# Performance work log

Measured on AMD Instinct MI355X. Metric: run time of the kernel, lower is better.

## Reference

```python
import jax, jax.numpy as jnp
import numpy as np

DIM = 2048
HID = 4096          # multiple_of*ceil(int(2*6144/3)/256)
STATE = 128
HEADS = 64
GROUPS = 1
CONV = 4
CHUNK = 256
HEAD_DIM = HID // HEADS            # 64
CONV_DIM = HID + 2 * GROUPS * STATE  # 4352
D_IN = 2 * HID + 2 * GROUPS * STATE + HEADS  # 8512


def setup_inputs() -> dict:
    key = jax.random.key(0)
    ks = jax.random.split(key, 8)
    x = jax.random.normal(ks[0], (1, 4096, DIM), dtype=jnp.float32)
    in_proj_w = jax.random.normal(ks[1], (D_IN, DIM), jnp.float32) * (DIM ** -0.5)
    conv_w = jax.random.normal(ks[2], (CONV_DIM, CONV), jnp.float32) * (CONV ** -0.5)
    # dt_bias init: log(expm1(uniform(dt_min, dt_max)))
    dt_bias = jnp.log(jnp.expm1(jax.random.uniform(ks[3], (HEADS,), jnp.float32, 0.001, 0.1)))
    # A_log init: log(uniform(A_init_min, A_init_max))
    A_log = jnp.log(jax.random.uniform(ks[4], (HEADS,), jnp.float32, 1.0, 16.0))
    D = jnp.ones((HEADS,), jnp.float32)
    norm_w = jnp.ones((HID,), jnp.float32)
    out_proj_w = jax.random.normal(ks[5], (DIM, HID), jnp.float32) * (HID ** -0.5)
    return dict(x=x, in_proj_w=in_proj_w, conv_w=conv_w, dt_bias=dt_bias,
                A_log=A_log, D=D, norm_w=norm_w, out_proj_w=out_proj_w)


def _causal_conv1d_silu(xBC, w):
    # xBC: (b, s, c); w: (c, k) depthwise causal conv, then SiLU
    b, s, c = xBC.shape
    k = w.shape[1]
    xp = jnp.pad(xBC, ((0, 0), (k - 1, 0), (0, 0)))
    out = xp[:, 0:s, :] * w[:, 0]
    for i in range(1, k):
        out = out + xp[:, i:i + s, :] * w[:, i]
    return jax.nn.silu(out)


def _ssd_chunk_scan(x, dt, A, B, C, D, chunk):
    # x: (b,s,h,p), dt: (b,s,h) post-softplus, A: (h,) negative, B,C: (b,s,g,n)
    b, s, h, p = x.shape
    g, n = B.shape[2], B.shape[3]
    c = s // chunk
    Bh = jnp.repeat(B, h // g, axis=2).reshape(b, c, chunk, h, n)
    Ch = jnp.repeat(C, h // g, axis=2).reshape(b, c, chunk, h, n)
    xr = x.reshape(b, c, chunk, h, p)
    dtr = dt.reshape(b, c, chunk, h)
    dA = dtr * A                      # (b,c,l,h)
    dAc = jnp.cumsum(dA, axis=2)      # (b,c,l,h)
    # intra-chunk (diagonal blocks): decay[i,j] = exp(dAc[i]-dAc[j]) for i>=j
    seg = dAc[:, :, :, None, :] - dAc[:, :, None, :, :]   # (b,c,l,l,h)
    mask = jnp.tril(jnp.ones((chunk, chunk), bool))
    Lmat = jnp.where(mask[None, None, :, :, None], jnp.exp(seg), 0.0)
    xdt = xr * dtr[..., None]         # dt-scaled inputs
    y_diag = jnp.einsum('bclhn,bcshn,bclsh,bcshp->bclhp', Ch, Bh, Lmat, xdt)
    # per-chunk end states
    dA_last = dAc[:, :, -1:, :]                       # (b,c,1,h)
    decay_states = jnp.exp(dA_last - dAc)             # (b,c,l,h)
    states = jnp.einsum('bclhn,bclh,bclhp->bchpn', Bh, decay_states, xdt)
    # inter-chunk recurrence
    chunk_decay = jnp.exp(dA_last[:, :, 0, :])        # (b,c,h)
    def step(carry, inp):
        dec, st = inp
        new = carry * dec[:, :, None, None] + st
        return new, carry
    init = jnp.zeros((b, h, p, n), x.dtype)
    _, prev = jax.lax.scan(step, init,
                           (jnp.moveaxis(chunk_decay, 1, 0), jnp.moveaxis(states, 1, 0)))
    prev = jnp.moveaxis(prev, 0, 1)                   # (b,c,h,p,n) state entering each chunk
    y_off = jnp.einsum('bclhn,bclh,bchpn->bclhp', Ch, jnp.exp(dAc), prev)
    y = (y_diag + y_off).reshape(b, s, h, p)
    return y + x * D[None, None, :, None]


def reference(x, in_proj_w, conv_w, dt_bias, A_log, D, norm_w, out_proj_w):
    b, s, _ = x.shape
    zxbcdt = x @ in_proj_w.T                          # (b,s,D_IN)
    z = zxbcdt[..., :HID]
    xBC = zxbcdt[..., HID:HID + CONV_DIM]
    dt = zxbcdt[..., HID + CONV_DIM:]                 # (b,s,heads)
    xBC = _causal_conv1d_silu(xBC, conv_w)
    xh = xBC[..., :HID].reshape(b, s, HEADS, HEAD_DIM)
    B = xBC[..., HID:HID + GROUPS * STATE].reshape(b, s, GROUPS, STATE)
    C = xBC[..., HID + GROUPS * STATE:].reshape(b, s, GROUPS, STATE)
    A = -jnp.exp(A_log)
    dt = jax.nn.softplus(dt + dt_bias)                # dt_softplus=True with dt_bias
    y = _ssd_chunk_scan(xh, dt, A, B, C, D, CHUNK)
    y = y.reshape(b, s, HID)
    y = y * jax.nn.silu(z)                            # gated
    y = y * jax.lax.rsqrt(jnp.mean(y * y, axis=-1, keepdims=True) + 1e-5) * norm_w
    return y @ out_proj_w.T
```

## Files before the change

### kernel.cpp

```cpp
#include <hip/hip_runtime.h>
#include <cstdint>
#include <cstddef>

#define SEQ      4096
#define DIMIN    2048
#define HID      4096
#define STATE    128
#define HEADS    64
#define HEAD_DIM 64
#define CONV_DIM 4352
#define D_IN     8512
#define WROWS    8576
#define XBCD_N   4480
#define CHUNK    256
#define NCHUNK   16

typedef __attribute__((ext_vector_type(8))) short short8;
typedef __attribute__((ext_vector_type(4))) float floatx4;
typedef __attribute__((ext_vector_type(4))) unsigned int uintx4;

#define AS1 __attribute__((address_space(1)))
#define AS3 __attribute__((address_space(3)))
__device__ __forceinline__ void gload_lds16(const void* g, void* l) {
    __builtin_amdgcn_global_load_lds((const AS1 unsigned int*)g, (AS3 unsigned int*)l, 16, 0, 0);
}

__device__ __forceinline__ unsigned short f2bf(float f) {
    union { float f; unsigned int u; } v; v.f = f;
    unsigned int r = v.u + 0x7FFFu + ((v.u >> 16) & 1u);
    return (unsigned short)(r >> 16);
}
__device__ __forceinline__ float bf2f(unsigned short u) {
    union { unsigned int u; float f; } v; v.u = ((unsigned int)u) << 16;
    return v.f;
}

__global__ void k_convert(const float* __restrict__ src, unsigned short* __restrict__ dst,
                          long n, long nsrc) {
    long i = (long)blockIdx.x * blockDim.x + threadIdx.x;
    if (i >= n) return;
    float v = (i < nsrc) ? src[i] : 0.f;
    dst[i] = f2bf(v);
}

#define BM 128
#define BN 128
#define BK 64

template <int BF16OUT>
__global__ __launch_bounds__(256) void k_gemm(
    const unsigned short* __restrict__ A, const unsigned short* __restrict__ B,
    void* __restrict__ Cout, int K, int ldc, float* __restrict__ aux, int auxc0)
{
    __shared__ __attribute__((aligned(16))) unsigned short As[BM * BK];
    __shared__ __attribute__((aligned(16))) unsigned short Bs[BN * BK];
    const int tid = threadIdx.x;

    const int GN = 8;
    const int nbx = gridDim.x, nby = gridDim.y;
    int flat = blockIdx.y * nbx + blockIdx.x;
    int group = flat / (GN * nby);
    int gw = min(GN, nbx - group * GN);
    int rem = flat - group * (GN * nby);
    int bn = group * GN + rem % gw;
    int bm = rem / gw;

    const int wid = tid >> 6, lane = tid & 63;
    const int wm = (wid >> 1) * 64, wn = (wid & 1) * 64;
    const int lrow = lane & 15;
    const int gk = lane >> 4;
    const int srow = lane >> 3;
    const int sgrp = (lane & 7) ^ (lane >> 3);

    floatx4 acc[4][4];
#pragma unroll
    for (int i = 0; i < 4; ++i)
#pragma unroll
        for (int j = 0; j < 4; ++j) acc[i][j] = (floatx4){0.f, 0.f, 0.f, 0.f};

    const long a_base = (long)bm * BM * K;
    const long b_base = (long)bn * BN * K;

    for (int k0 = 0; k0 < K; k0 += BK) {
        const unsigned short* Ak = A + a_base + k0;
        const unsigned short* Bk = B + b_base + k0;
#pragma unroll
        for (int i = 0; i < 4; ++i) {
            int rbase = wid * 32 + i * 8;
            gload_lds16(Ak + (long)(rbase + srow) * K + sgrp * 8, &As[rbase * BK]);
            gload_lds16(Bk + (long)(rbase + srow) * K + sgrp * 8, &Bs[rbase * BK]);
        }
        __syncthreads();
#pragma unroll
        for (int kk = 0; kk < BK; kk += 32) {
            const int slot8 = (((kk >> 3) + gk) ^ (lrow & 7)) * 8;
            short8 af[4], bfr[4];
#pragma unroll
            for (int i = 0; i < 4; ++i)
                af[i] = *(const short8*)&As[(wm + i * 16 + lrow) * BK + slot8];
#pragma unroll
            for (int j = 0; j < 4; ++j)
                bfr[j] = *(const short8*)&Bs[(wn + j * 16 + lrow) * BK + slot8];
#pragma unroll
            for (int i = 0; i < 4; ++i)
#pragma unroll
                for (int j = 0; j < 4; ++j)
                    acc[i][j] = __builtin_amdgcn_mfma_f32_16x16x32_bf16(af[i], bfr[j], acc[i][j], 0, 0, 0);
        }
        __syncthreads();
    }
    const int rcol = lane & 15;
    const int rrow = (lane >> 4) * 4;
#pragma unroll
    for (int i = 0; i < 4; ++i)
#pragma unroll
        for (int j = 0; j < 4; ++j) {
            int col = bn * BN + wn + j * 16 + rcol;
#pragma unroll
            for (int r = 0; r < 4; ++r) {
                int row = bm * BM + wm + i * 16 + rrow + r;
                float v = acc[i][j][r];
                if (BF16OUT) {
                    ((unsigned short*)Cout)[(long)row * ldc + col] = f2bf(v);
                    if (aux && col >= auxc0 && col < auxc0 + 64)
                        aux[(long)row * 64 + (col - auxc0)] = v;
                } else {
                    ((float*)Cout)[(long)row * ldc + col] = v;
                }
            }
        }
}

__global__ void k_conv(const unsigned short* __restrict__ xbcd, const float* __restrict__ convw,
                       unsigned short* __restrict__ xc) {
    long i = (long)blockIdx.x * 256 + threadIdx.x;
    if (i >= (long)SEQ * CONV_DIM) return;
    int c = (int)(i % CONV_DIM);
    int s = (int)(i / CONV_DIM);
    float w0 = convw[c * 4 + 0], w1 = convw[c * 4 + 1];
    float w2 = convw[c * 4 + 2], w3 = convw[c * 4 + 3];
    float acc = bf2f(xbcd[(long)s * XBCD_N + c]) * w3;
    if (s >= 1) acc += bf2f(xbcd[(long)(s - 1) * XBCD_N + c]) * w2;
    if (s >= 2) acc += bf2f(xbcd[(long)(s - 2) * XBCD_N + c]) * w1;
    if (s >= 3) acc += bf2f(xbcd[(long)(s - 3) * XBCD_N + c]) * w0;
    float sl = acc / (1.f + __expf(-acc));
    xc[i] = f2bf(sl);
}

__global__ __launch_bounds__(256) void k_dt(const float* __restrict__ dtraw,
        const float* __restrict__ dt_bias, const float* __restrict__ A_log,
        float* __restrict__ dtv, float* __restrict__ dAc, float* __restrict__ dAlast)
{
    int c = blockIdx.x, h = blockIdx.y;
    int l = threadIdx.x;
    __shared__ float sh[CHUNK];
    float v = dtraw[(long)(c * CHUNK + l) * 64 + h] + dt_bias[h];
    float dt = (v > 20.f) ? v : log1pf(__expf(v));
    float Ah = -__expf(A_log[h]);
    float dA = dt * Ah;
    sh[l] = dA;
    __syncthreads();
    float x = dA;
#pragma unroll
    for (int off = 1; off < CHUNK; off <<= 1) {
        float t = (l >= off) ? sh[l - off] : 0.f;
        __syncthreads();
        x += t;
        sh[l] = x;
        __syncthreads();
    }
    dtv[(long)(c * CHUNK + l) * HEADS + h] = dt;
    dAc[(long)(c * CHUNK + l) * HEADS + h] = x;
    if (l == CHUNK - 1) dAlast[c * HEADS + h] = x;
}

__global__ __launch_bounds__(256) void k_G(const unsigned short* __restrict__ xc, float* __restrict__ G) {
    int c = blockIdx.x, l = blockIdx.y;
    int s = threadIdx.x;
    __shared__ float Csh[STATE];
    if (s < STATE) Csh[s] = bf2f(xc[(long)(c * CHUNK + l) * CONV_DIM + HID + STATE + s]);
    __syncthreads();
    const unsigned short* Brow = xc + (long)(c * CHUNK + s) * CONV_DIM + HID;
    float acc = 0.f;
#pragma unroll
    for (int n = 0; n < STATE; n += 8) {
        short8 b8 = *(const short8*)&Brow[n];
#pragma unroll
        for (int j = 0; j < 8; ++j)
            acc += Csh[n + j] * bf2f((unsigned short)b8[j]);
    }
    G[((long)c * CHUNK + l) * CHUNK + s] = acc;
}

__global__ __launch_bounds__(256) void k_states(
    const unsigned short* __restrict__ xc, const float* __restrict__ dtv,
    const float* __restrict__ dAc, const float* __restrict__ dAlast,
    float* __restrict__ states)
{
    int c = blockIdx.x, h = blockIdx.y;
    int t = threadIdx.x;
    __shared__ float xs[64][64];
    __shared__ float dA_sh[CHUNK], dt_sh[CHUNK];
    long base_s = (long)c * CHUNK;
    dA_sh[t] = dAc[(base_s + t) * HEADS + h];
    dt_sh[t] = dtv[(base_s + t) * HEADS + h];
    __syncthreads();
    float dAl = dAlast[c * HEADS + h];
    int p0 = t >> 5;
    int n0 = t & 31;
    float acc[8][4];
#pragma unroll
    for (int ip = 0; ip < 8; ++ip)
#pragma unroll
        for (int j = 0; j < 4; ++j) acc[ip][j] = 0.f;

    for (int lb = 0; lb < 4; ++lb) {
#pragma unroll
        for (int i = 0; i < 16; ++i) {
            int e = t + i * 256;
            int r = e >> 6, pcol = e & 63;
            float ds = __expf(dAl - dA_sh[lb * 64 + r]) * dt_sh[lb * 64 + r];
            xs[r][pcol] = bf2f(xc[(base_s + lb * 64 + r) * CONV_DIM + h * HEAD_DIM + pcol]) * ds;
        }
        __syncthreads();
        for (int lp = 0; lp < 64; ++lp) {
            const unsigned short* Brow = xc + (base_s + lb * 64 + lp) * CONV_DIM + HID;
            float bv[4];
#pragma unroll
            for (int j = 0; j < 4; ++j) bv[j] = bf2f(Brow[n0 + 32 * j]);
#pragma unroll
            for (int ip = 0; ip < 8; ++ip) {
                float xv = xs[lp][p0 + 8 * ip];
#pragma unroll
                for (int j = 0; j < 4; ++j) acc[ip][j] += xv * bv[j];
            }
        }
        __syncthreads();
    }
    float* Sb = states + (long)(c * HEADS + h) * HEAD_DIM * STATE;
#pragma unroll
    for (int ip = 0; ip < 8; ++ip)
#pragma unroll
        for (int j = 0; j < 4; ++j)
            Sb[(p0 + 8 * ip) * STATE + n0 + 32 * j] = acc[ip][j];
}

__global__ void k_scan(float* __restrict__ states, const float* __restrict__ dAlast) {
    int t = blockIdx.x * 256 + threadIdx.x;
    if (t >= HEADS * HEAD_DIM * STATE) return;
    int h = t >> 13;
    const long stride = (long)HEADS * HEAD_DIM * STATE;
    float carry = 0.f;
    for (int c = 0; c < NCHUNK; ++c) {
        float s = states[c * stride + t];
        float dec = __expf(dAlast[c * HEADS + h]);
        states[c * stride + t] = carry;
        carry = carry * dec + s;
    }
}

#define XDTS 264
#define PVS  136
__global__ __launch_bounds__(256, 3) void k_ssd_y(
    const unsigned short* __restrict__ xc, const float* __restrict__ G,
    const float* __restrict__ dtv, const float* __restrict__ dAc,
    const float* __restrict__ prev, const float* __restrict__ Dp,
    unsigned short* __restrict__ y)
{
    __shared__ __attribute__((aligned(16))) unsigned short xdtT[64 * XDTS];
    __shared__ __attribute__((aligned(16))) unsigned short pvB[64 * PVS];
    __shared__ float dA_sh[CHUNK];
    __shared__ float dt_sh[CHUNK];
    const int c = blockIdx.x, h = blockIdx.y;
    const int t = threadIdx.x;
    const int w = t >> 6, lane = t & 63;
    const long base_s = (long)c * CHUNK;

    dA_sh[t] = dAc[(base_s + t) * HEADS + h];
    dt_sh[t] = dtv[(base_s + t) * HEADS + h];
    __syncthreads();

    {
        const float* Pb = prev + (long)(c * HEADS + h) * HEAD_DIM * STATE;
#pragma unroll
        for (int i = 0; i < 32; ++i) {
            int e = t + i * 256;
            int p = e >> 7, n = e & 127;
            pvB[p * PVS + n] = f2bf(Pb[e]);
        }
    }
#pragma unroll
    for (int i = 0; i < 64; ++i) {
        int e = t + i * 256;
        int p = e & 63, s = e >> 6;
        float v = bf2f(xc[(base_s + s) * CONV_DIM + h * HEAD_DIM + p]) * dt_sh[s];
        xdtT[p * XDTS + s] = f2bf(v);
    }
    __syncthreads();

    floatx4 acc[4][4];
#pragma unroll
    for (int i = 0; i < 4; ++i)
#pragma unroll
        for (int j = 0; j < 4; ++j) acc[i][j] = (floatx4){0.f, 0.f, 0.f, 0.f};

    const int lrow = lane & 15;
    const int kgrp = (lane >> 4) * 8;
    float myA[4], eAl[4];
#pragma unroll
    for (int i = 0; i < 4; ++i) {
        int l = w * 64 + i * 16 + lrow;
        myA[i] = dA_sh[l];
        eAl[i] = __expf(myA[i]);
    }

    for (int k0 = 0; k0 < STATE; k0 += 32) {
        short8 af[4], bfr[4];
#pragma unroll
        for (int i = 0; i < 4; ++i) {
            int l = w * 64 + i * 16 + lrow;
            union { short8 v; unsigned short u[8]; } r, o;
            r.v = *(const short8*)&xc[(base_s + l) * CONV_DIM + (HID + STATE) + k0 + kgrp];
#pragma unroll
            for (int j = 0; j < 8; ++j) o.u[j] = f2bf(bf2f(r.u[j]) * eAl[i]);
            af[i] = o.v;
        }
#pragma unroll
        for (int j = 0; j < 4; ++j)
            bfr[j] = *(const short8*)&pvB[(j * 16 + lrow) * PVS + k0 + kgrp];
#pragma unroll
        for (int i = 0; i < 4; ++i)
#pragma unroll
            for (int j = 0; j < 4; ++j)
                acc[i][j] = __builtin_amdgcn_mfma_f32_16x16x32_bf16(af[i], bfr[j], acc[i][j], 0, 0, 0);
    }

    for (int k0 = 0; k0 < (w + 1) * 64; k0 += 32) {
        short8 af[4], bfr[4];
#pragma unroll
        for (int i = 0; i < 4; ++i) {
            int l = w * 64 + i * 16 + lrow;
            const float* Gp = G + (base_s + l) * (long)CHUNK + k0 + kgrp;
            float4 g0 = *(const float4*)Gp;
            float4 g1 = *(const float4*)(Gp + 4);
            float ga[8] = {g0.x, g0.y, g0.z, g0.w, g1.x, g1.y, g1.z, g1.w};
            union { short8 v; unsigned short u[8]; } o;
#pragma unroll
            for (int j = 0; j < 8; ++j) {
                int s = k0 + kgrp + j;
                float e = __expf(fminf(myA[i] - dA_sh[s], 0.f));
                float m = (s <= l) ? ga[j] * e : 0.f;
                o.u[j] = f2bf(m);
            }
            af[i] = o.v;
        }
#pragma unroll
        for (int j = 0; j < 4; ++j)
            bfr[j] = *(const short8*)&xdtT[(j * 16 + lrow) * XDTS + k0 + kgrp];
#pragma unroll
        for (int i = 0; i < 4; ++i)
#pragma unroll
            for (int j = 0; j < 4; ++j)
                acc[i][j] = __builtin_amdgcn_mfma_f32_16x16x32_bf16(af[i], bfr[j], acc[i][j], 0, 0, 0);
    }

    const float Dh = Dp[h];
    const int rrow = (lane >> 4) * 4;
#pragma unroll
    for (int i = 0; i < 4; ++i)
#pragma unroll
        for (int j = 0; j < 4; ++j) {
            int p = j * 16 + lrow;
#pragma unroll
            for (int r = 0; r < 4; ++r) {
                int l = w * 64 + i * 16 + rrow + r;
                float v = acc[i][j][r] + Dh * bf2f(xc[(base_s + l) * CONV_DIM + h * HEAD_DIM + p]);
                y[(base_s + l) * (long)HID + h * HEAD_DIM + p] = f2bf(v);
            }
        }
}

__global__ __launch_bounds__(256) void k_norm(
    const unsigned short* __restrict__ y, const unsigned short* __restrict__ z,
    const float* __restrict__ norm_w, unsigned short* __restrict__ yb)
{
    int s = blockIdx.x;
    int t = threadIdx.x;
    const unsigned short* yrow = y + (long)s * HID;
    const unsigned short* zrow = z + (long)s * HID;
    float vals[16];
    float ss = 0.f;
#pragma unroll
    for (int i = 0; i < 16; ++i) {
        int j = t + i * 256;
        float yv = bf2f(yrow[j]);
        float zv = bf2f(zrow[j]);
        float g = yv * (zv / (1.f + __expf(-zv)));
        vals[i] = g;
        ss += g * g;
    }
#pragma unroll
    for (int off = 32; off > 0; off >>= 1) ss += __shfl_down(ss, off);
    __shared__ float wsum[4];
    int lane = t & 63, wid = t >> 6;
    if (lane == 0) wsum[wid] = ss;
    __syncthreads();
    float total = wsum[0] + wsum[1] + wsum[2] + wsum[3];
    float scale = rsqrtf(total / HID + 1e-5f);
#pragma unroll
    for (int i = 0; i < 16; ++i) {
        int j = t + i * 256;
        yb[(long)s * HID + j] = f2bf(vals[i] * scale * norm_w[j]);
    }
}

extern "C" void kernel_launch(void* const* d_in, const int* in_sizes, int n_in,
                              void* d_out, int out_size, void* d_ws, size_t ws_size,
                              hipStream_t stream) {
    const float* x          = (const float*)d_in[0];
    const float* in_proj_w  = (const float*)d_in[1];
    const float* conv_w     = (const float*)d_in[2];
    const float* dt_bias    = (const float*)d_in[3];
    const float* A_log      = (const float*)d_in[4];
    const float* Dp         = (const float*)d_in[5];
    const float* norm_w     = (const float*)d_in[6];
    const float* out_proj_w = (const float*)d_in[7];
    char* ws = (char*)d_ws;

    const size_t off_xb    = 0;
    const size_t off_wbin  = off_xb    + (size_t)SEQ * DIMIN * 2;
    const size_t off_xbcd  = off_wbin  + (size_t)WROWS * DIMIN * 2;
    const size_t off_xc    = off_xbcd  + (size_t)SEQ * XBCD_N * 2;
    const size_t off_dtraw = off_xc    + (size_t)SEQ * CONV_DIM * 2;
    const size_t off_dtv   = off_dtraw + (size_t)SEQ * 64 * 4;
    const size_t off_dAc   = off_dtv   + (size_t)SEQ * HEADS * 4;
    const size_t off_dAl   = off_dAc   + (size_t)SEQ * HEADS * 4;
    const size_t off_G     = off_dAl   + (size_t)NCHUNK * HEADS * 4;
    const size_t needed    = off_G     + (size_t)NCHUNK * CHUNK * CHUNK * 4;
    if (ws_size < needed) return;

    unsigned short* xb    = (unsigned short*)(ws + off_xb);
    unsigned short* wbin  = (unsigned short*)(ws + off_wbin);
    unsigned short* xbcd  = (unsigned short*)(ws + off_xbcd);
    unsigned short* xc    = (unsigned short*)(ws + off_xc);
    float* dtraw = (float*)(ws + off_dtraw);
    float* dtv   = (float*)(ws + off_dtv);
    float* dAc   = (float*)(ws + off_dAc);
    float* dAl   = (float*)(ws + off_dAl);
    float* G     = (float*)(ws + off_G);

    float* states      = (float*)d_out;
    unsigned short* z  = (unsigned short*)d_out;
    unsigned short* y  = xbcd;
    unsigned short* yb = xc;
    unsigned short* wob = wbin;

    { long n = (long)SEQ * DIMIN;
      k_convert<<<(unsigned)((n + 255) / 256), 256, 0, stream>>>(x, xb, n, n); }
    { long n = (long)WROWS * DIMIN, nsrc = (long)D_IN * DIMIN;
      k_convert<<<(unsigned)((n + 255) / 256), 256, 0, stream>>>(in_proj_w, wbin, n, nsrc); }
    k_gemm<1><<<dim3(XBCD_N / BN, SEQ / BM), 256, 0, stream>>>(
        xb, wbin + (size_t)HID * DIMIN, (void*)xbcd, DIMIN, XBCD_N, dtraw, 4352);
    { long n = (long)SEQ * CONV_DIM;
      k_conv<<<(unsigned)((n + 255) / 256), 256, 0, stream>>>(xbcd, conv_w, xc); }
    k_dt<<<dim3(NCHUNK, HEADS), 256, 0, stream>>>(dtraw, dt_bias, A_log, dtv, dAc, dAl);
    k_G<<<dim3(NCHUNK, CHUNK), 256, 0, stream>>>(xc, G);
    k_states<<<dim3(NCHUNK, HEADS), 256, 0, stream>>>(xc, dtv, dAc, dAl, states);
    k_scan<<<(HEADS * HEAD_DIM * STATE) / 256, 256, 0, stream>>>(states, dAl);
    k_ssd_y<<<dim3(NCHUNK, HEADS), 256, 0, stream>>>(xc, G, dtv, dAc, states, Dp, y);
    k_gemm<1><<<dim3(HID / BN, SEQ / BM), 256, 0, stream>>>(
        xb, wbin, (void*)z, DIMIN, HID, nullptr, 0);
    k_norm<<<SEQ, 256, 0, stream>>>(y, z, norm_w, yb);
    { long n = (long)DIMIN * HID;
      k_convert<<<(unsigned)((n + 255) / 256), 256, 0, stream>>>(out_proj_w, wob, n, n); }
    k_gemm<0><<<dim3(DIMIN / BN, SEQ / BM), 256, 0, stream>>>(
        yb, wob, d_out, HID, DIMIN, nullptr, 0);
}
```

Baseline: 766.7 us.

## Replace GEMM with 256x256 double-buffered pipelined kernel and split-K out_proj

Replaces the 128x128 single-buffered bf16 MFMA GEMM with a 256x256 tile, 512-thread kernel. It double-buffers LDS with interleaved global-to-LDS staging, raises wave priority around the MFMA blocks, and remaps workgroups to XCDs. The out_proj GEMM is split across K into two halves, with the second partial written to workspace and summed by a new add kernel. This targets low MFMA utilisation and load latency in all three GEMMs, and fills the GPU for the small out_proj grid. The cost is more LDS per block, an extra pass over the output, and tight barrier and vmcnt choreography that could misorder if counts are wrong.

```diff
diff --git a/kernel.cpp b/kernel.cpp
--- a/kernel.cpp
+++ b/kernel.cpp
@@ -17,7 +17,6 @@
 
 typedef __attribute__((ext_vector_type(8))) short short8;
 typedef __attribute__((ext_vector_type(4))) float floatx4;
-typedef __attribute__((ext_vector_type(4))) unsigned int uintx4;
 
 #define AS1 __attribute__((address_space(1)))
 #define AS3 __attribute__((address_space(3)))
@@ -43,92 +42,191 @@
     dst[i] = f2bf(v);
 }
 
-#define BM 128
-#define BN 128
-#define BK 64
+#define GBM 256
+#define GBN 256
+#define GBK 64
 
 template <int BF16OUT>
-__global__ __launch_bounds__(256) void k_gemm(
+__global__ __launch_bounds__(512, 2) void k_gemm256(
     const unsigned short* __restrict__ A, const unsigned short* __restrict__ B,
-    void* __restrict__ Cout, int K, int ldc, float* __restrict__ aux, int auxc0)
+    void* __restrict__ Cout, float* __restrict__ Cpart,
+    int Kloop, int ldk, int Nvalid, int ldc,
+    float* __restrict__ aux, int auxc0)
 {
-    __shared__ __attribute__((aligned(16))) unsigned short As[BM * BK];
-    __shared__ __attribute__((aligned(16))) unsigned short Bs[BN * BK];
-    const int tid = threadIdx.x;
-
-    const int GN = 8;
+    __shared__ __attribute__((aligned(16))) unsigned short As[2][GBM * GBK];
+    __shared__ __attribute__((aligned(16))) unsigned short Bs[2][GBN * GBK];
+
+    const int tid  = threadIdx.x;
+    const int wid  = tid >> 6, lane = tid & 63;
+    const int wm   = (wid >> 2) * 128;
+    const int wn   = (wid & 3) * 64;
+
     const int nbx = gridDim.x, nby = gridDim.y;
-    int flat = blockIdx.y * nbx + blockIdx.x;
-    int group = flat / (GN * nby);
-    int gw = min(GN, nbx - group * GN);
-    int rem = flat - group * (GN * nby);
-    int bn = group * GN + rem % gw;
-    int bm = rem / gw;
-
-    const int wid = tid >> 6, lane = tid & 63;
-    const int wm = (wid >> 1) * 64, wn = (wid & 1) * 64;
+    const int nwg = nbx * nby * (int)gridDim.z;
+    int flat = ((int)blockIdx.z * nby + blockIdx.y) * nbx + blockIdx.x;
+    int q = nwg >> 3, r = nwg & 7;
+    int xcd = flat & 7, loc = flat >> 3;
+    int f2 = (xcd < r ? xcd * (q + 1) : r * (q + 1) + (xcd - r) * q) + loc;
+    int bz  = f2 / (nbx * nby);
+    int rm2 = f2 - bz * nbx * nby;
+    int bm  = rm2 / nbx;
+    int bn  = rm2 % nbx;
+
+    const unsigned short* Ag = A + (long)bm * GBM * ldk + (long)bz * Kloop;
+    const unsigned short* Bg = B + (long)bn * GBN * ldk + (long)bz * Kloop;
+
+    const int s_r  = lane >> 3;
+    const int s_kg = (lane & 7) ^ s_r;
+
     const int lrow = lane & 15;
-    const int gk = lane >> 4;
-    const int srow = lane >> 3;
-    const int sgrp = (lane & 7) ^ (lane >> 3);
-
-    floatx4 acc[4][4];
-#pragma unroll
-    for (int i = 0; i < 4; ++i)
+    const int gk   = lane >> 4;
+
+    floatx4 acc[8][4];
+#pragma unroll
+    for (int i = 0; i < 8; ++i)
 #pragma unroll
         for (int j = 0; j < 4; ++j) acc[i][j] = (floatx4){0.f, 0.f, 0.f, 0.f};
 
-    const long a_base = (long)bm * BM * K;
-    const long b_base = (long)bn * BN * K;
-
-    for (int k0 = 0; k0 < K; k0 += BK) {
-        const unsigned short* Ak = A + a_base + k0;
-        const unsigned short* Bk = B + b_base + k0;
-#pragma unroll
-        for (int i = 0; i < 4; ++i) {
-            int rbase = wid * 32 + i * 8;
-            gload_lds16(Ak + (long)(rbase + srow) * K + sgrp * 8, &As[rbase * BK]);
-            gload_lds16(Bk + (long)(rbase + srow) * K + sgrp * 8, &Bs[rbase * BK]);
-        }
-        __syncthreads();
-#pragma unroll
-        for (int kk = 0; kk < BK; kk += 32) {
-            const int slot8 = (((kk >> 3) + gk) ^ (lrow & 7)) * 8;
-            short8 af[4], bfr[4];
-#pragma unroll
-            for (int i = 0; i < 4; ++i)
-                af[i] = *(const short8*)&As[(wm + i * 16 + lrow) * BK + slot8];
-#pragma unroll
-            for (int j = 0; j < 4; ++j)
-                bfr[j] = *(const short8*)&Bs[(wn + j * 16 + lrow) * BK + slot8];
-#pragma unroll
-            for (int i = 0; i < 4; ++i)
-#pragma unroll
-                for (int j = 0; j < 4; ++j)
-                    acc[i][j] = __builtin_amdgcn_mfma_f32_16x16x32_bf16(af[i], bfr[j], acc[i][j], 0, 0, 0);
-        }
-        __syncthreads();
-    }
-    const int rcol = lane & 15;
-    const int rrow = (lane >> 4) * 4;
-#pragma unroll
-    for (int i = 0; i < 4; ++i)
-#pragma unroll
-        for (int j = 0; j < 4; ++j) {
-            int col = bn * BN + wn + j * 16 + rcol;
-#pragma unroll
-            for (int r = 0; r < 4; ++r) {
-                int row = bm * BM + wm + i * 16 + rrow + r;
-                float v = acc[i][j][r];
+    short8 aLo[4][2], aHi[4][2], bF[4][2];
+
+    unsigned short* As0 = As[0]; unsigned short* Bs0 = Bs[0];
+    unsigned short* As1 = As[1]; unsigned short* Bs1 = Bs[1];
+
+    auto STAGE = [&](unsigned short* Ad, unsigned short* Bd, int tt, int p) {
+        long k0 = (long)tt * GBK;
+        if (k0 + GBK > Kloop) k0 = 0;
+        const int seg = p * 8 + wid;
+        const long ro = (long)(seg * 8 + s_r) * ldk + k0 + s_kg * 8;
+        gload_lds16(Ag + ro, Ad + seg * 512);
+        gload_lds16(Bg + ro, Bd + seg * 512);
+    };
+    auto LDA_ = [&](unsigned short* Asu, int m, int ks) -> short8 {
+        int row  = wm + m * 16 + lrow;
+        int slot = (gk + ks * 4) ^ (lrow & 7);
+        return *(const short8*)&Asu[row * 64 + slot * 8];
+    };
+    auto LDB_ = [&](unsigned short* Bsu, int n, int ks) -> short8 {
+        int row  = wn + n * 16 + lrow;
+        int slot = (gk + ks * 4) ^ (lrow & 7);
+        return *(const short8*)&Bsu[row * 64 + slot * 8];
+    };
+
+#pragma unroll
+    for (int p = 0; p < 4; ++p) STAGE(As0, Bs0, 0, p);
+    STAGE(As1, Bs1, 1, 0);
+    STAGE(As1, Bs1, 1, 1);
+    asm volatile("s_waitcnt vmcnt(4)" ::: "memory");
+    __builtin_amdgcn_s_barrier();
+    asm volatile("" ::: "memory");
+
+    const int nk = Kloop / GBK;
+
+    auto tile_step = [&](unsigned short* Asu, unsigned short* Bsu,
+                         unsigned short* AsN, unsigned short* BsN, int t) {
+#pragma unroll
+        for (int m = 0; m < 4; ++m) { aLo[m][0] = LDA_(Asu, m, 0); aLo[m][1] = LDA_(Asu, m, 1); }
+#pragma unroll
+        for (int n = 0; n < 2; ++n) { bF[n][0] = LDB_(Bsu, n, 0); bF[n][1] = LDB_(Bsu, n, 1); }
+        STAGE(AsN, BsN, t + 1, 2);
+        __builtin_amdgcn_s_barrier();
+        asm volatile("" ::: "memory");
+        __builtin_amdgcn_s_setprio(1);
+#pragma unroll
+        for (int m = 0; m < 4; ++m)
+#pragma unroll
+            for (int n = 0; n < 2; ++n)
+#pragma unroll
+                for (int ks = 0; ks < 2; ++ks)
+                    acc[m][n] = __builtin_amdgcn_mfma_f32_16x16x32_bf16(aLo[m][ks], bF[n][ks], acc[m][n], 0, 0, 0);
+        __builtin_amdgcn_s_setprio(0);
+        __builtin_amdgcn_s_barrier();
+        asm volatile("" ::: "memory");
+#pragma unroll
+        for (int n = 2; n < 4; ++n) { bF[n][0] = LDB_(Bsu, n, 0); bF[n][1] = LDB_(Bsu, n, 1); }
+        STAGE(AsN, BsN, t + 1, 3);
+        __builtin_amdgcn_s_barrier();
+        asm volatile("" ::: "memory");
+        __builtin_amdgcn_s_setprio(1);
+#pragma unroll
+        for (int m = 0; m < 4; ++m)
+#pragma unroll
+            for (int n = 2; n < 4; ++n)
+#pragma unroll
+                for (int ks = 0; ks < 2; ++ks)
+                    acc[m][n] = __builtin_amdgcn_mfma_f32_16x16x32_bf16(aLo[m][ks], bF[n][ks], acc[m][n], 0, 0, 0);
+        __builtin_amdgcn_s_setprio(0);
+        __builtin_amdgcn_s_barrier();
+        asm volatile("" ::: "memory");
+#pragma unroll
+        for (int m = 0; m < 4; ++m) { aHi[m][0] = LDA_(Asu, m + 4, 0); aHi[m][1] = LDA_(Asu, m + 4, 1); }
+        STAGE(Asu, Bsu, t + 2, 0);
+        __builtin_amdgcn_s_barrier();
+        asm volatile("" ::: "memory");
+        __builtin_amdgcn_s_setprio(1);
+#pragma unroll
+        for (int m = 0; m < 4; ++m)
+#pragma unroll
+            for (int n = 2; n < 4; ++n)
+#pragma unroll
+                for (int ks = 0; ks < 2; ++ks)
+                    acc[m + 4][n] = __builtin_amdgcn_mfma_f32_16x16x32_bf16(aHi[m][ks], bF[n][ks], acc[m + 4][n], 0, 0, 0);
+        __builtin_amdgcn_s_setprio(0);
+        __builtin_amdgcn_s_barrier();
+        asm volatile("" ::: "memory");
+        STAGE(Asu, Bsu, t + 2, 1);
+        __builtin_amdgcn_s_barrier();
+        asm volatile("" ::: "memory");
+        __builtin_amdgcn_s_setprio(1);
+#pragma unroll
+        for (int m = 0; m < 4; ++m)
+#pragma unroll
+            for (int n = 0; n < 2; ++n)
+#pragma unroll
+                for (int ks = 0; ks < 2; ++ks)
+                    acc[m + 4][n] = __builtin_amdgcn_mfma_f32_16x16x32_bf16(aHi[m][ks], bF[n][ks], acc[m + 4][n], 0, 0, 0);
+        __builtin_amdgcn_s_setprio(0);
+        asm volatile("s_waitcnt vmcnt(4)" ::: "memory");
+        __builtin_amdgcn_s_barrier();
+        asm volatile("" ::: "memory");
+    };
+
+#pragma unroll 1
+    for (int t = 0; t < nk; t += 2) {
+        tile_step(As0, Bs0, As1, Bs1, t);
+        tile_step(As1, Bs1, As0, Bs0, t + 1);
+    }
+
+    const int rcol = lane & 15, rrow = (lane >> 4) * 4;
+#pragma unroll
+    for (int m = 0; m < 8; ++m)
+#pragma unroll
+        for (int n = 0; n < 4; ++n) {
+            const int colb = bn * GBN + wn + n * 16;
+            if (colb >= Nvalid) continue;
+            const int col = colb + rcol;
+#pragma unroll
+            for (int r2 = 0; r2 < 4; ++r2) {
+                const int row = bm * GBM + wm + m * 16 + rrow + r2;
+                float v = acc[m][n][r2];
                 if (BF16OUT) {
                     ((unsigned short*)Cout)[(long)row * ldc + col] = f2bf(v);
                     if (aux && col >= auxc0 && col < auxc0 + 64)
                         aux[(long)row * 64 + (col - auxc0)] = v;
                 } else {
-                    ((float*)Cout)[(long)row * ldc + col] = v;
+                    float* op = bz ? Cpart : (float*)Cout;
+                    op[(long)row * ldc + col] = v;
                 }
             }
         }
+}
+
+__global__ void k_add(float* __restrict__ dst, const float* __restrict__ src, long n4) {
+    long i = (long)blockIdx.x * blockDim.x + threadIdx.x;
+    if (i >= n4) return;
+    float4 a = ((const float4*)src)[i];
+    float4 d = ((float4*)dst)[i];
+    d.x += a.x; d.y += a.y; d.z += a.z; d.w += a.w;
+    ((float4*)dst)[i] = d;
 }
 
 __global__ void k_conv(const unsigned short* __restrict__ xbcd, const float* __restrict__ convw,
@@ -454,13 +552,15 @@
     unsigned short* y  = xbcd;
     unsigned short* yb = xc;
     unsigned short* wob = wbin;
+    float* gpart = (float*)(ws + off_xbcd);
 
     { long n = (long)SEQ * DIMIN;
       k_convert<<<(unsigned)((n + 255) / 256), 256, 0, stream>>>(x, xb, n, n); }
     { long n = (long)WROWS * DIMIN, nsrc = (long)D_IN * DIMIN;
       k_convert<<<(unsigned)((n + 255) / 256), 256, 0, stream>>>(in_proj_w, wbin, n, nsrc); }
-    k_gemm<1><<<dim3(XBCD_N / BN, SEQ / BM), 256, 0, stream>>>(
-        xb, wbin + (size_t)HID * DIMIN, (void*)xbcd, DIMIN, XBCD_N, dtraw, 4352);
+    k_gemm256<1><<<dim3((XBCD_N + GBN - 1) / GBN, SEQ / GBM, 1), 512, 0, stream>>>(
+        xb, wbin + (size_t)HID * DIMIN, (void*)xbcd, nullptr,
+        DIMIN, DIMIN, XBCD_N, XBCD_N, dtraw, 4352);
     { long n = (long)SEQ * CONV_DIM;
       k_conv<<<(unsigned)((n + 255) / 256), 256, 0, stream>>>(xbcd, conv_w, xc); }
     k_dt<<<dim3(NCHUNK, HEADS), 256, 0, stream>>>(dtraw, dt_bias, A_log, dtv, dAc, dAl);
@@ -468,11 +568,13 @@
     k_states<<<dim3(NCHUNK, HEADS), 256, 0, stream>>>(xc, dtv, dAc, dAl, states);
     k_scan<<<(HEADS * HEAD_DIM * STATE) / 256, 256, 0, stream>>>(states, dAl);
     k_ssd_y<<<dim3(NCHUNK, HEADS), 256, 0, stream>>>(xc, G, dtv, dAc, states, Dp, y);
-    k_gemm<1><<<dim3(HID / BN, SEQ / BM), 256, 0, stream>>>(
-        xb, wbin, (void*)z, DIMIN, HID, nullptr, 0);
+    k_gemm256<1><<<dim3(HID / GBN, SEQ / GBM, 1), 512, 0, stream>>>(
+        xb, wbin, (void*)z, nullptr, DIMIN, DIMIN, HID, HID, nullptr, 0);
     k_norm<<<SEQ, 256, 0, stream>>>(y, z, norm_w, yb);
     { long n = (long)DIMIN * HID;
       k_convert<<<(unsigned)((n + 255) / 256), 256, 0, stream>>>(out_proj_w, wob, n, n); }
-    k_gemm<0><<<dim3(DIMIN / BN, SEQ / BM), 256, 0, stream>>>(
-        yb, wob, d_out, HID, DIMIN, nullptr, 0);
-}
+    k_gemm256<0><<<dim3(DIMIN / GBN, SEQ / GBM, 2), 512, 0, stream>>>(
+        yb, wob, d_out, gpart, HID / 2, HID, DIMIN, DIMIN, nullptr, 0);
+    k_add<<<(unsigned)(((long)SEQ * DIMIN / 4 + 255) / 256), 256, 0, stream>>>(
+        (float*)d_out, gpart, (long)SEQ * DIMIN / 4);
+}
```

Result: no change. 759.9 us (-0.9%).
